# Kernel tuning notes

Measured on AMD Instinct MI355X. Metric: run time of the kernel, lower is better.

## Reference

```python
import jax, jax.numpy as jnp
import numpy as np

IN_F = 256
OUT_F = 256
ALPHA = 0.2  # leaky-relu slope
NEG_INF = -9e15


def setup_inputs() -> dict:
    key = jax.random.key(0)
    ks = jax.random.split(key, 8)
    N_e, N_kc = 10000, 2000
    exercise_h = jax.random.normal(ks[0], (N_e, IN_F), dtype=jnp.float32)
    kc_h = jax.random.normal(ks[1], (N_kc, IN_F), dtype=jnp.float32)
    adj = jax.random.randint(ks[2], (N_e, N_kc), 0, 2, dtype=jnp.int32)
    # parameters (kaiming-ish scaling)
    W1 = jax.random.normal(ks[3], (IN_F, OUT_F), dtype=jnp.float32) * np.sqrt(2.0 / IN_F)
    E = jax.random.normal(ks[4], (IN_F, OUT_F), dtype=jnp.float32) * np.sqrt(2.0 / IN_F)
    a = jax.random.normal(ks[5], (2 * OUT_F, 1), dtype=jnp.float32) * np.sqrt(2.0 / (2 * OUT_F))
    rd_w = jax.random.normal(ks[6], (OUT_F, 2 * OUT_F), dtype=jnp.float32) * np.sqrt(2.0 / (2 * OUT_F))
    rd_b = jnp.zeros((OUT_F,), dtype=jnp.float32)
    return {"exercise_h": exercise_h, "kc_h": kc_h, "adj": adj,
            "W1": W1, "E": E, "a": a, "rd_w": rd_w, "rd_b": rd_b}


def reference(exercise_h, kc_h, adj, W1, E, a, rd_w, rd_b):
    kc_Wh = kc_h @ W1            # [N_kc, D]
    ex_Wh = exercise_h @ W1      # [N_e, D]
    # a . concat(ex_Wh_i, kc_Wh_j) == a1.ex_Wh_i + a2.kc_Wh_j  (avoids [N_e,N_kc,2D] tensor)
    a1 = a[:OUT_F, 0]
    a2 = a[OUT_F:, 0]
    e = jax.nn.leaky_relu((ex_Wh @ a1)[:, None] + (kc_Wh @ a2)[None, :], negative_slope=ALPHA)  # [N_e, N_kc]
    logits = jnp.where(adj > 0, e, jnp.float32(NEG_INF))
    attention = jax.nn.softmax(logits, axis=1)
    new_kc = attention @ kc_Wh           # [N_e, D]
    ex_Eh = exercise_h @ E               # [N_e, D]
    feat = jnp.concatenate([new_kc, new_kc * ex_Eh], axis=1)  # [N_e, 2D]
    out = feat @ rd_w.T + rd_b
    return jax.nn.elu(out)
```

## Files before the change

kernel.cpp:

```cpp
#include <hip/hip_runtime.h>

#define N_E 10000
#define N_KC 2000
#define ALPHA 0.2f

typedef __attribute__((ext_vector_type(8))) short short8;
typedef __attribute__((ext_vector_type(4))) float f32x4;

__device__ float g_w1a1[256];
__device__ float g_t[2048];
__device__ __align__(16) unsigned short g_W1T_pk[16 * 8 * 512];
__device__ __align__(16) unsigned short g_ET_pk[16 * 8 * 512];
__device__ __align__(16) unsigned short g_rdw_pk[16 * 16 * 512];
__device__ __align__(16) unsigned short g_kcWh_pk[16 * 64 * 512];

__device__ __forceinline__ unsigned short f2bf(float f) {
  union { float f; unsigned int u; } v; v.f = f;
  unsigned int r = v.u + 0x7FFFu + ((v.u >> 16) & 1u);
  return (unsigned short)(r >> 16);
}

__device__ __forceinline__ void cvt_store4(float4 v, unsigned short* dst) {
  ushort4 o;
  o.x = f2bf(v.x); o.y = f2bf(v.y); o.z = f2bf(v.z); o.w = f2bf(v.w);
  *reinterpret_cast<ushort4*>(dst) = o;
}

__global__ __launch_bounds__(256) void prep_kernel(
    const float* __restrict__ W1, const float* __restrict__ E,
    const float* __restrict__ a, const float* __restrict__ rd_w) {
  int b = blockIdx.x, tid = threadIdx.x;
  if (b < 32) {
#pragma unroll
    for (int s2 = 0; s2 < 2; ++s2) {
      int sId = b * 512 + tid + s2 * 256;
      int ct = sId >> 10, rem = sId & 1023;
      int kt = rem >> 6, lane = rem & 63;
      int g = lane >> 4, r = lane & 15;
      const float* src = rd_w + (size_t)(ct * 16 + r) * 512 + kt * 32 + g * 8;
      unsigned short* dst = g_rdw_pk + (size_t)sId * 8;
      cvt_store4(*(const float4*)src, dst);
      cvt_store4(*(const float4*)(src + 4), dst + 4);
    }
  } else if (b < 48) {
#pragma unroll
    for (int s2 = 0; s2 < 2; ++s2) {
      int sId = (b - 32) * 512 + tid + s2 * 256;
      int ct = sId >> 9, rem = sId & 511;
      int kt = rem >> 6, lane = rem & 63;
      int g = lane >> 4, r = lane & 15;
      int col = ct * 16 + r, k = kt * 32 + g * 8;
      unsigned short* dst = g_W1T_pk + (size_t)sId * 8;
      ushort4 o0, o1;
      o0.x = f2bf(W1[(k + 0) * 256 + col]); o0.y = f2bf(W1[(k + 1) * 256 + col]);
      o0.z = f2bf(W1[(k + 2) * 256 + col]); o0.w = f2bf(W1[(k + 3) * 256 + col]);
      o1.x = f2bf(W1[(k + 4) * 256 + col]); o1.y = f2bf(W1[(k + 5) * 256 + col]);
      o1.z = f2bf(W1[(k + 6) * 256 + col]); o1.w = f2bf(W1[(k + 7) * 256 + col]);
      *(ushort4*)dst = o0; *(ushort4*)(dst + 4) = o1;
    }
  } else if (b < 64) {
#pragma unroll
    for (int s2 = 0; s2 < 2; ++s2) {
      int sId = (b - 48) * 512 + tid + s2 * 256;
      int ct = sId >> 9, rem = sId & 511;
      int kt = rem >> 6, lane = rem & 63;
      int g = lane >> 4, r = lane & 15;
      int col = ct * 16 + r, k = kt * 32 + g * 8;
      unsigned short* dst = g_ET_pk + (size_t)sId * 8;
      ushort4 o0, o1;
      o0.x = f2bf(E[(k + 0) * 256 + col]); o0.y = f2bf(E[(k + 1) * 256 + col]);
      o0.z = f2bf(E[(k + 2) * 256 + col]); o0.w = f2bf(E[(k + 3) * 256 + col]);
      o1.x = f2bf(E[(k + 4) * 256 + col]); o1.y = f2bf(E[(k + 5) * 256 + col]);
      o1.z = f2bf(E[(k + 6) * 256 + col]); o1.w = f2bf(E[(k + 7) * 256 + col]);
      *(ushort4*)dst = o0; *(ushort4*)(dst + 4) = o1;
    }
  } else if (b == 64) {
    float acc = 0.f;
    for (int q = 0; q < 64; ++q) {
      float4 wv = *(const float4*)(W1 + (size_t)tid * 256 + q * 4);
      float4 a4 = *(const float4*)(a + q * 4);
      acc += wv.x * a4.x + wv.y * a4.y + wv.z * a4.z + wv.w * a4.w;
    }
    g_w1a1[tid] = acc;
  } else {
    for (int idx = tid; idx < 16 * 2 * 512; idx += 256) {
      int ct = idx >> 10, rem = idx & 1023;
      int kt = 62 + (rem >> 9), off = rem & 511;
      g_kcWh_pk[((size_t)ct * 64 + kt) * 512 + off] = 0;
    }
    if (tid < 48) g_t[2000 + tid] = 0.f;
  }
}

__global__ __launch_bounds__(256) void kc_mfma_kernel(
    const float* __restrict__ kc_h, const float* __restrict__ a) {
  __shared__ float tred[4][4][4];
  int tid = threadIdx.x, lane = tid & 63, w = tid >> 6;
  int r = lane & 15, g = lane >> 4;
  int j0 = blockIdx.x * 16;
  f32x4 acc[4] = {{0.f,0.f,0.f,0.f},{0.f,0.f,0.f,0.f},
                  {0.f,0.f,0.f,0.f},{0.f,0.f,0.f,0.f}};
  for (int kk = 0; kk < 8; ++kk) {
    int k = kk * 32 + g * 8;
    const float* src = kc_h + (size_t)(j0 + r) * 256 + k;
    float4 x0 = *(const float4*)src, x1 = *(const float4*)(src + 4);
    short8 af = {(short)f2bf(x0.x), (short)f2bf(x0.y), (short)f2bf(x0.z),
                 (short)f2bf(x0.w), (short)f2bf(x1.x), (short)f2bf(x1.y),
                 (short)f2bf(x1.z), (short)f2bf(x1.w)};
#pragma unroll
    for (int n = 0; n < 4; ++n) {
      short8 bf = *(const short8*)(g_W1T_pk + ((size_t)(w * 4 + n) * 8 + kk) *
                                                  512 + lane * 8);
      acc[n] = __builtin_amdgcn_mfma_f32_16x16x32_bf16(af, bf, acc[n], 0, 0, 0);
    }
  }
  int j = j0 + g * 4;
  int kt = j >> 5, lsub = ((j >> 3) & 3) * 16 + r, sub = (g & 1) * 4;
#pragma unroll
  for (int n = 0; n < 4; ++n) {
    int ct = w * 4 + n;
    ushort4 o;
    o.x = f2bf(acc[n][0]); o.y = f2bf(acc[n][1]);
    o.z = f2bf(acc[n][2]); o.w = f2bf(acc[n][3]);
    *reinterpret_cast<ushort4*>(
        g_kcWh_pk + ((size_t)ct * 64 + kt) * 512 + lsub * 8 + sub) = o;
  }
  float a2v[4];
#pragma unroll
  for (int n = 0; n < 4; ++n) a2v[n] = a[256 + w * 64 + n * 16 + r];
  float tp[4];
#pragma unroll
  for (int q = 0; q < 4; ++q)
    tp[q] = acc[0][q] * a2v[0] + acc[1][q] * a2v[1] + acc[2][q] * a2v[2] +
            acc[3][q] * a2v[3];
#pragma unroll
  for (int off = 1; off < 16; off <<= 1)
#pragma unroll
    for (int q = 0; q < 4; ++q) tp[q] += __shfl_xor(tp[q], off, 64);
  if (r == 0)
#pragma unroll
    for (int q = 0; q < 4; ++q) tred[w][g][q] = tp[q];
  __syncthreads();
  if (tid < 16)
    g_t[j0 + tid] = tred[0][tid >> 2][tid & 3] + tred[1][tid >> 2][tid & 3] +
                    tred[2][tid >> 2][tid & 3] + tred[3][tid >> 2][tid & 3];
}

#define PSTR 136
#define FST 536
__global__ __launch_bounds__(512, 4) void main_kernel(
    const float* __restrict__ exh, const int* __restrict__ adj,
    const float* __restrict__ rd_b, float* __restrict__ out) {
  __shared__ __align__(16) unsigned char smem[41984];
  __shared__ float ds_part[8][32];
  __shared__ float red32[32];
  float* t_s = (float*)smem;
  unsigned short* p_s = (unsigned short*)(smem + 8192);
  unsigned short* exh_pk_s = (unsigned short*)(smem + 25600);
  unsigned short* feat_s = (unsigned short*)smem;

  int tid = threadIdx.x, w = tid >> 6, lane = tid & 63;
  int r = lane & 15, g = lane >> 4;
  int i0 = blockIdx.x * 32;
  int mh = w >> 2;
  int kw = w & 3;

  ((float4*)t_s)[tid] = ((const float4*)g_t)[tid];
  {
    const float* wsrc = g_w1a1 + w * 32 + g * 8;
    float4 w0 = *(const float4*)wsrc, w1 = *(const float4*)(wsrc + 4);
    float sp[2];
#pragma unroll
    for (int m = 0; m < 2; ++m) {
      int row = i0 + m * 16 + r; row = row < N_E ? row : N_E - 1;
      const float* xsrc = exh + (size_t)row * 256 + w * 32 + g * 8;
      float4 x0 = *(const float4*)xsrc, x1 = *(const float4*)(xsrc + 4);
      unsigned short* dst = exh_pk_s + m * 4096 + w * 512 + lane * 8;
      cvt_store4(x0, dst); cvt_store4(x1, dst + 4);
      sp[m] = x0.x * w0.x + x0.y * w0.y + x0.z * w0.z + x0.w * w0.w +
              x1.x * w1.x + x1.y * w1.y + x1.z * w1.z + x1.w * w1.w;
      sp[m] += __shfl_xor(sp[m], 16, 64);
      sp[m] += __shfl_xor(sp[m], 32, 64);
    }
    if (lane < 16) { ds_part[w][lane] = sp[0]; ds_part[w][16 + lane] = sp[1]; }
  }
  __syncthreads();
  if (tid < 32) {
    float sv = 0.f;
#pragma unroll
    for (int ww = 0; ww < 8; ++ww) sv += ds_part[ww][tid];
    red32[tid] = sv;
  }
  __syncthreads();
  float sv = red32[mh * 16 + r];
  int grow = i0 + mh * 16 + r; grow = grow < N_E ? grow : N_E - 1;
  const int* arow = adj + (size_t)grow * N_KC;

  f32x4 accP[2][2] = {{{0.f,0.f,0.f,0.f},{0.f,0.f,0.f,0.f}},
                      {{0.f,0.f,0.f,0.f},{0.f,0.f,0.f,0.f}}};
  float dsum = 0.f;

  auto gen = [&](int c) {
    int kk = c * 4 + kw;
    int c0 = kk * 32 + g * 8;
    int4 pk = {0, 0, 0, 0};
    if (kk < 63 && c0 < N_KC) {
      int4 a0 = *(const int4*)(arow + c0);
      int4 a1 = *(const int4*)(arow + c0 + 4);
      float4 t0 = *(const float4*)(t_s + c0);
      float4 t1 = *(const float4*)(t_s + c0 + 4);
      float tv[8] = {t0.x, t0.y, t0.z, t0.w, t1.x, t1.y, t1.z, t1.w};
      int av[8] = {a0.x, a0.y, a0.z, a0.w, a1.x, a1.y, a1.z, a1.w};
      unsigned ub[8];
#pragma unroll
      for (int j = 0; j < 8; ++j) {
        float x = sv + tv[j];
        float lx = fmaxf(x, ALPHA * x);
        float pv = (av[j] > 0) ? __expf(lx) : 0.f;
        dsum += pv;
        ub[j] = __float_as_uint(pv) + 0x8000u;
      }
      pk.x = (int)((ub[0] >> 16) | (ub[1] & 0xFFFF0000u));
      pk.y = (int)((ub[2] >> 16) | (ub[3] & 0xFFFF0000u));
      pk.z = (int)((ub[4] >> 16) | (ub[5] & 0xFFFF0000u));
      pk.w = (int)((ub[6] >> 16) | (ub[7] & 0xFFFF0000u));
    }
    *(int4*)(p_s + ((size_t)(c & 1) * 32 + mh * 16 + r) * PSTR + kw * 32 +
             g * 8) = pk;
  };

  auto mfma_chunk = [&](int c) {
    const unsigned short* pb = p_s + (size_t)(c & 1) * 32 * PSTR;
    const unsigned short* bb0 =
        g_kcWh_pk + ((size_t)(w * 2 + 0) * 64 + c * 4) * 512 + lane * 8;
    const unsigned short* bb1 =
        g_kcWh_pk + ((size_t)(w * 2 + 1) * 64 + c * 4) * 512 + lane * 8;
    short8 b0 = *(const short8*)bb0;
    short8 b1 = *(const short8*)bb1;
#pragma unroll
    for (int u = 0; u < 4; ++u) {
      short8 a0 = *(const short8*)(pb + (size_t)r * PSTR + u * 32 + g * 8);
      short8 a1 = *(const short8*)(pb + (size_t)(16 + r) * PSTR + u * 32 + g * 8);
      short8 nb0 = b0, nb1 = b1;
      if (u < 3) {
        nb0 = *(const short8*)(bb0 + (u + 1) * 512);
        nb1 = *(const short8*)(bb1 + (u + 1) * 512);
      }
      accP[0][0] = __builtin_amdgcn_mfma_f32_16x16x32_bf16(a0, b0, accP[0][0], 0, 0, 0);
      accP[1][0] = __builtin_amdgcn_mfma_f32_16x16x32_bf16(a1, b0, accP[1][0], 0, 0, 0);
      accP[0][1] = __builtin_amdgcn_mfma_f32_16x16x32_bf16(a0, b1, accP[0][1], 0, 0, 0);
      accP[1][1] = __builtin_amdgcn_mfma_f32_16x16x32_bf16(a1, b1, accP[1][1], 0, 0, 0);
      b0 = nb0; b1 = nb1;
    }
  };

  gen(0);
  __syncthreads();
  for (int c = 1; c < 16; ++c) {
    gen(c);
    mfma_chunk(c - 1);
    __syncthreads();
  }
  mfma_chunk(15);

  dsum += __shfl_xor(dsum, 16, 64);
  dsum += __shfl_xor(dsum, 32, 64);
  if (lane < 16) {
    ds_part[w][mh * 16 + lane] = dsum;
    ds_part[w][(1 - mh) * 16 + lane] = 0.f;
  }

  f32x4 accE[2][2] = {{{0.f,0.f,0.f,0.f},{0.f,0.f,0.f,0.f}},
                      {{0.f,0.f,0.f,0.f},{0.f,0.f,0.f,0.f}}};
#pragma unroll
  for (int kk = 0; kk < 8; ++kk) {
    short8 a0 = *(const short8*)(exh_pk_s + kk * 512 + lane * 8);
    short8 a1 = *(const short8*)(exh_pk_s + 4096 + kk * 512 + lane * 8);
#pragma unroll
    for (int n = 0; n < 2; ++n) {
      short8 bf = *(const short8*)(g_ET_pk + ((size_t)(w * 2 + n) * 8 + kk) *
                                                 512 + lane * 8);
      accE[0][n] = __builtin_amdgcn_mfma_f32_16x16x32_bf16(a0, bf, accE[0][n], 0, 0, 0);
      accE[1][n] = __builtin_amdgcn_mfma_f32_16x16x32_bf16(a1, bf, accE[1][n], 0, 0, 0);
    }
  }
  __syncthreads();
  if (tid < 32) {
    float s = 0.f;
#pragma unroll
    for (int ww = 0; ww < 8; ++ww) s += ds_part[ww][tid];
    red32[tid] = 1.f / fmaxf(s, 1e-30f);
  }
  __syncthreads();

  int c0e = w * 32;
#pragma unroll
  for (int m = 0; m < 2; ++m)
#pragma unroll
    for (int n = 0; n < 2; ++n) {
      int col = c0e + n * 16 + r;
#pragma unroll
      for (int q = 0; q < 4; ++q) {
        int row = m * 16 + g * 4 + q;
        float nk = accP[m][n][q] * red32[row];
        feat_s[(size_t)row * FST + col] = f2bf(nk);
        feat_s[(size_t)row * FST + 256 + col] = f2bf(nk * accE[m][n][q]);
      }
    }
  __syncthreads();

  f32x4 accO[2][2] = {{{0.f,0.f,0.f,0.f},{0.f,0.f,0.f,0.f}},
                      {{0.f,0.f,0.f,0.f},{0.f,0.f,0.f,0.f}}};
#pragma unroll
  for (int kt = 0; kt < 16; ++kt) {
    int k = kt * 32 + g * 8;
    short8 a0 = *(const short8*)(feat_s + (size_t)r * FST + k);
    short8 a1 = *(const short8*)(feat_s + (size_t)(16 + r) * FST + k);
#pragma unroll
    for (int n = 0; n < 2; ++n) {
      short8 bf = *(const short8*)(g_rdw_pk + ((size_t)(w * 2 + n) * 16 + kt) *
                                                  512 + lane * 8);
      accO[0][n] = __builtin_amdgcn_mfma_f32_16x16x32_bf16(a0, bf, accO[0][n], 0, 0, 0);
      accO[1][n] = __builtin_amdgcn_mfma_f32_16x16x32_bf16(a1, bf, accO[1][n], 0, 0, 0);
    }
  }
#pragma unroll
  for (int m = 0; m < 2; ++m) {
    if (i0 + m * 16 >= N_E) continue;
#pragma unroll
    for (int n = 0; n < 2; ++n) {
      int col = c0e + n * 16 + r;
      float bias = rd_b[col];
#pragma unroll
      for (int q = 0; q < 4; ++q) {
        int row = i0 + m * 16 + g * 4 + q;
        float x = accO[m][n][q] + bias;
        float res = x > 0.f ? x : (__expf(x) - 1.f);
        out[(size_t)row * 256 + col] = res;
      }
    }
  }
}

extern "C" void kernel_launch(void* const* d_in, const int* in_sizes, int n_in,
                              void* d_out, int out_size, void* d_ws,
                              size_t ws_size, hipStream_t stream) {
  const float* exh  = (const float*)d_in[0];
  const float* kc_h = (const float*)d_in[1];
  const int*   adj  = (const int*)d_in[2];
  const float* W1   = (const float*)d_in[3];
  const float* E    = (const float*)d_in[4];
  const float* a    = (const float*)d_in[5];
  const float* rd_w = (const float*)d_in[6];
  const float* rd_b = (const float*)d_in[7];
  float* out = (float*)d_out;

  prep_kernel<<<66, 256, 0, stream>>>(W1, E, a, rd_w);
  kc_mfma_kernel<<<N_KC / 16, 256, 0, stream>>>(kc_h, a);
  main_kernel<<<(N_E + 31) / 32, 512, 0, stream>>>(exh, adj, rd_b, out);
}
```

Baseline: 184.2 us.

## Shrink main kernel row tile to 16 and software-prefetch adjacency loads

Each block of the main kernel now handles 16 exercise rows instead of 32, doubling the grid and raising the launch-bounds occupancy target from 4 to 8 blocks. Every wave now walks the full K range in 8 chunks of 256 columns instead of the previous two-half split. The adjacency int4 loads are prefetched into registers one chunk ahead, so global-load latency overlaps the exp/pack and MFMA work. The cost is that the kcWh, E and rd_w B-fragments are each reused by only one 16-row M-tile, so global/L2 traffic for those weights per output row roughly doubles. The row clamp for N_E is also removed, which is safe only because 10000 divides evenly by 16.

```diff
diff --git a/kernel.cpp b/kernel.cpp
--- a/kernel.cpp
+++ b/kernel.cpp
@@ -146,71 +146,64 @@
                     tred[2][tid >> 2][tid & 3] + tred[3][tid >> 2][tid & 3];
 }
 
-#define PSTR 136
+#define PSTR 264
 #define FST 536
-__global__ __launch_bounds__(512, 4) void main_kernel(
+__global__ __launch_bounds__(512, 8) void main_kernel(
     const float* __restrict__ exh, const int* __restrict__ adj,
     const float* __restrict__ rd_b, float* __restrict__ out) {
-  __shared__ __align__(16) unsigned char smem[41984];
-  __shared__ float ds_part[8][32];
-  __shared__ float red32[32];
+  __shared__ __align__(16) unsigned char smem[33280];
+  __shared__ float ds_part[8][16];
+  __shared__ float red16[16];
   float* t_s = (float*)smem;
   unsigned short* p_s = (unsigned short*)(smem + 8192);
-  unsigned short* exh_pk_s = (unsigned short*)(smem + 25600);
+  unsigned short* exh_pk_s = (unsigned short*)(smem + 25088);
   unsigned short* feat_s = (unsigned short*)smem;
 
   int tid = threadIdx.x, w = tid >> 6, lane = tid & 63;
   int r = lane & 15, g = lane >> 4;
-  int i0 = blockIdx.x * 32;
-  int mh = w >> 2;
-  int kw = w & 3;
+  int i0 = blockIdx.x * 16;
+
+  const int* arow = adj + (size_t)(i0 + r) * N_KC;
+
+  int4 pa0 = *(const int4*)(arow + w * 32 + g * 8);
+  int4 pa1 = *(const int4*)(arow + w * 32 + g * 8 + 4);
 
   ((float4*)t_s)[tid] = ((const float4*)g_t)[tid];
   {
     const float* wsrc = g_w1a1 + w * 32 + g * 8;
     float4 w0 = *(const float4*)wsrc, w1 = *(const float4*)(wsrc + 4);
-    float sp[2];
-#pragma unroll
-    for (int m = 0; m < 2; ++m) {
-      int row = i0 + m * 16 + r; row = row < N_E ? row : N_E - 1;
-      const float* xsrc = exh + (size_t)row * 256 + w * 32 + g * 8;
-      float4 x0 = *(const float4*)xsrc, x1 = *(const float4*)(xsrc + 4);
-      unsigned short* dst = exh_pk_s + m * 4096 + w * 512 + lane * 8;
-      cvt_store4(x0, dst); cvt_store4(x1, dst + 4);
-      sp[m] = x0.x * w0.x + x0.y * w0.y + x0.z * w0.z + x0.w * w0.w +
-              x1.x * w1.x + x1.y * w1.y + x1.z * w1.z + x1.w * w1.w;
-      sp[m] += __shfl_xor(sp[m], 16, 64);
-      sp[m] += __shfl_xor(sp[m], 32, 64);
-    }
-    if (lane < 16) { ds_part[w][lane] = sp[0]; ds_part[w][16 + lane] = sp[1]; }
-  }
-  __syncthreads();
-  if (tid < 32) {
-    float sv = 0.f;
-#pragma unroll
-    for (int ww = 0; ww < 8; ++ww) sv += ds_part[ww][tid];
-    red32[tid] = sv;
-  }
-  __syncthreads();
-  float sv = red32[mh * 16 + r];
-  int grow = i0 + mh * 16 + r; grow = grow < N_E ? grow : N_E - 1;
-  const int* arow = adj + (size_t)grow * N_KC;
-
-  f32x4 accP[2][2] = {{{0.f,0.f,0.f,0.f},{0.f,0.f,0.f,0.f}},
-                      {{0.f,0.f,0.f,0.f},{0.f,0.f,0.f,0.f}}};
+    const float* xsrc = exh + (size_t)(i0 + r) * 256 + w * 32 + g * 8;
+    float4 x0 = *(const float4*)xsrc, x1 = *(const float4*)(xsrc + 4);
+    unsigned short* dst = exh_pk_s + w * 512 + lane * 8;
+    cvt_store4(x0, dst); cvt_store4(x1, dst + 4);
+    float sp = x0.x * w0.x + x0.y * w0.y + x0.z * w0.z + x0.w * w0.w +
+               x1.x * w1.x + x1.y * w1.y + x1.z * w1.z + x1.w * w1.w;
+    sp += __shfl_xor(sp, 16, 64);
+    sp += __shfl_xor(sp, 32, 64);
+    if (lane < 16) ds_part[w][lane] = sp;
+  }
+  __syncthreads();
+  if (tid < 16) {
+    float s = 0.f;
+#pragma unroll
+    for (int ww = 0; ww < 8; ++ww) s += ds_part[ww][tid];
+    red16[tid] = s;
+  }
+  __syncthreads();
+  float sv = red16[r];
+
+  f32x4 accP[2] = {{0.f,0.f,0.f,0.f},{0.f,0.f,0.f,0.f}};
   float dsum = 0.f;
 
-  auto gen = [&](int c) {
-    int kk = c * 4 + kw;
+  auto gen = [&](int c, int4 a0v, int4 a1v) {
+    int kk = c * 8 + w;
     int c0 = kk * 32 + g * 8;
     int4 pk = {0, 0, 0, 0};
     if (kk < 63 && c0 < N_KC) {
-      int4 a0 = *(const int4*)(arow + c0);
-      int4 a1 = *(const int4*)(arow + c0 + 4);
       float4 t0 = *(const float4*)(t_s + c0);
       float4 t1 = *(const float4*)(t_s + c0 + 4);
       float tv[8] = {t0.x, t0.y, t0.z, t0.w, t1.x, t1.y, t1.z, t1.w};
-      int av[8] = {a0.x, a0.y, a0.z, a0.w, a1.x, a1.y, a1.z, a1.w};
+      int av[8] = {a0v.x, a0v.y, a0v.z, a0v.w, a1v.x, a1v.y, a1v.z, a1v.w};
       unsigned ub[8];
 #pragma unroll
       for (int j = 0; j < 8; ++j) {
@@ -225,119 +218,98 @@
       pk.z = (int)((ub[4] >> 16) | (ub[5] & 0xFFFF0000u));
       pk.w = (int)((ub[6] >> 16) | (ub[7] & 0xFFFF0000u));
     }
-    *(int4*)(p_s + ((size_t)(c & 1) * 32 + mh * 16 + r) * PSTR + kw * 32 +
-             g * 8) = pk;
+    *(int4*)(p_s + ((size_t)((c & 1) * 16 + r)) * PSTR + w * 32 + g * 8) = pk;
   };
 
   auto mfma_chunk = [&](int c) {
-    const unsigned short* pb = p_s + (size_t)(c & 1) * 32 * PSTR;
-    const unsigned short* bb0 =
-        g_kcWh_pk + ((size_t)(w * 2 + 0) * 64 + c * 4) * 512 + lane * 8;
-    const unsigned short* bb1 =
-        g_kcWh_pk + ((size_t)(w * 2 + 1) * 64 + c * 4) * 512 + lane * 8;
-    short8 b0 = *(const short8*)bb0;
-    short8 b1 = *(const short8*)bb1;
-#pragma unroll
-    for (int u = 0; u < 4; ++u) {
-      short8 a0 = *(const short8*)(pb + (size_t)r * PSTR + u * 32 + g * 8);
-      short8 a1 = *(const short8*)(pb + (size_t)(16 + r) * PSTR + u * 32 + g * 8);
-      short8 nb0 = b0, nb1 = b1;
-      if (u < 3) {
-        nb0 = *(const short8*)(bb0 + (u + 1) * 512);
-        nb1 = *(const short8*)(bb1 + (u + 1) * 512);
+    const unsigned short* pb = p_s + (size_t)(c & 1) * 16 * PSTR;
+    const unsigned short* bb =
+        g_kcWh_pk + ((size_t)(w * 2) * 64 + c * 8) * 512 + lane * 8;
+#pragma unroll
+    for (int u = 0; u < 8; ++u) {
+      short8 av = *(const short8*)(pb + (size_t)r * PSTR + u * 32 + g * 8);
+      short8 b0 = *(const short8*)(bb + u * 512);
+      short8 b1 = *(const short8*)(bb + 64 * 512 + u * 512);
+      accP[0] = __builtin_amdgcn_mfma_f32_16x16x32_bf16(av, b0, accP[0], 0, 0, 0);
+      accP[1] = __builtin_amdgcn_mfma_f32_16x16x32_bf16(av, b1, accP[1], 0, 0, 0);
+    }
+  };
+
+  int4 na0 = {0, 0, 0, 0}, na1 = {0, 0, 0, 0};
+  for (int c = 0; c < 8; ++c) {
+    if (c < 7) {
+      int kk = (c + 1) * 8 + w, c0 = kk * 32 + g * 8;
+      if (kk < 63 && c0 < N_KC) {
+        na0 = *(const int4*)(arow + c0);
+        na1 = *(const int4*)(arow + c0 + 4);
       }
-      accP[0][0] = __builtin_amdgcn_mfma_f32_16x16x32_bf16(a0, b0, accP[0][0], 0, 0, 0);
-      accP[1][0] = __builtin_amdgcn_mfma_f32_16x16x32_bf16(a1, b0, accP[1][0], 0, 0, 0);
-      accP[0][1] = __builtin_amdgcn_mfma_f32_16x16x32_bf16(a0, b1, accP[0][1], 0, 0, 0);
-      accP[1][1] = __builtin_amdgcn_mfma_f32_16x16x32_bf16(a1, b1, accP[1][1], 0, 0, 0);
-      b0 = nb0; b1 = nb1;
-    }
-  };
-
-  gen(0);
-  __syncthreads();
-  for (int c = 1; c < 16; ++c) {
-    gen(c);
-    mfma_chunk(c - 1);
+    }
+    gen(c, pa0, pa1);
+    if (c > 0) mfma_chunk(c - 1);
     __syncthreads();
-  }
-  mfma_chunk(15);
+    pa0 = na0; pa1 = na1;
+  }
+  mfma_chunk(7);
 
   dsum += __shfl_xor(dsum, 16, 64);
   dsum += __shfl_xor(dsum, 32, 64);
-  if (lane < 16) {
-    ds_part[w][mh * 16 + lane] = dsum;
-    ds_part[w][(1 - mh) * 16 + lane] = 0.f;
-  }
-
-  f32x4 accE[2][2] = {{{0.f,0.f,0.f,0.f},{0.f,0.f,0.f,0.f}},
-                      {{0.f,0.f,0.f,0.f},{0.f,0.f,0.f,0.f}}};
+  if (lane < 16) ds_part[w][lane] = dsum;
+
+  f32x4 accE[2] = {{0.f,0.f,0.f,0.f},{0.f,0.f,0.f,0.f}};
 #pragma unroll
   for (int kk = 0; kk < 8; ++kk) {
     short8 a0 = *(const short8*)(exh_pk_s + kk * 512 + lane * 8);
-    short8 a1 = *(const short8*)(exh_pk_s + 4096 + kk * 512 + lane * 8);
 #pragma unroll
     for (int n = 0; n < 2; ++n) {
       short8 bf = *(const short8*)(g_ET_pk + ((size_t)(w * 2 + n) * 8 + kk) *
                                                  512 + lane * 8);
-      accE[0][n] = __builtin_amdgcn_mfma_f32_16x16x32_bf16(a0, bf, accE[0][n], 0, 0, 0);
-      accE[1][n] = __builtin_amdgcn_mfma_f32_16x16x32_bf16(a1, bf, accE[1][n], 0, 0, 0);
-    }
-  }
-  __syncthreads();
-  if (tid < 32) {
+      accE[n] = __builtin_amdgcn_mfma_f32_16x16x32_bf16(a0, bf, accE[n], 0, 0, 0);
+    }
+  }
+  __syncthreads();
+  if (tid < 16) {
     float s = 0.f;
 #pragma unroll
     for (int ww = 0; ww < 8; ++ww) s += ds_part[ww][tid];
-    red32[tid] = 1.f / fmaxf(s, 1e-30f);
-  }
-  __syncthreads();
-
-  int c0e = w * 32;
-#pragma unroll
-  for (int m = 0; m < 2; ++m)
-#pragma unroll
-    for (int n = 0; n < 2; ++n) {
-      int col = c0e + n * 16 + r;
-#pragma unroll
-      for (int q = 0; q < 4; ++q) {
-        int row = m * 16 + g * 4 + q;
-        float nk = accP[m][n][q] * red32[row];
-        feat_s[(size_t)row * FST + col] = f2bf(nk);
-        feat_s[(size_t)row * FST + 256 + col] = f2bf(nk * accE[m][n][q]);
-      }
-    }
-  __syncthreads();
-
-  f32x4 accO[2][2] = {{{0.f,0.f,0.f,0.f},{0.f,0.f,0.f,0.f}},
-                      {{0.f,0.f,0.f,0.f},{0.f,0.f,0.f,0.f}}};
+    red16[tid] = 1.f / fmaxf(s, 1e-30f);
+  }
+  __syncthreads();
+
+#pragma unroll
+  for (int n = 0; n < 2; ++n) {
+    int col = w * 32 + n * 16 + r;
+#pragma unroll
+    for (int q = 0; q < 4; ++q) {
+      int row = g * 4 + q;
+      float nk = accP[n][q] * red16[row];
+      feat_s[(size_t)row * FST + col] = f2bf(nk);
+      feat_s[(size_t)row * FST + 256 + col] = f2bf(nk * accE[n][q]);
+    }
+  }
+  __syncthreads();
+
+  f32x4 accO[2] = {{0.f,0.f,0.f,0.f},{0.f,0.f,0.f,0.f}};
 #pragma unroll
   for (int kt = 0; kt < 16; ++kt) {
     int k = kt * 32 + g * 8;
     short8 a0 = *(const short8*)(feat_s + (size_t)r * FST + k);
-    short8 a1 = *(const short8*)(feat_s + (size_t)(16 + r) * FST + k);
 #pragma unroll
     for (int n = 0; n < 2; ++n) {
       short8 bf = *(const short8*)(g_rdw_pk + ((size_t)(w * 2 + n) * 16 + kt) *
                                                   512 + lane * 8);
-      accO[0][n] = __builtin_amdgcn_mfma_f32_16x16x32_bf16(a0, bf, accO[0][n], 0, 0, 0);
-      accO[1][n] = __builtin_amdgcn_mfma_f32_16x16x32_bf16(a1, bf, accO[1][n], 0, 0, 0);
-    }
-  }
-#pragma unroll
-  for (int m = 0; m < 2; ++m) {
-    if (i0 + m * 16 >= N_E) continue;
-#pragma unroll
-    for (int n = 0; n < 2; ++n) {
-      int col = c0e + n * 16 + r;
-      float bias = rd_b[col];
-#pragma unroll
-      for (int q = 0; q < 4; ++q) {
-        int row = i0 + m * 16 + g * 4 + q;
-        float x = accO[m][n][q] + bias;
-        float res = x > 0.f ? x : (__expf(x) - 1.f);
-        out[(size_t)row * 256 + col] = res;
-      }
+      accO[n] = __builtin_amdgcn_mfma_f32_16x16x32_bf16(a0, bf, accO[n], 0, 0, 0);
+    }
+  }
+#pragma unroll
+  for (int n = 0; n < 2; ++n) {
+    int col = w * 32 + n * 16 + r;
+    float bias = rd_b[col];
+#pragma unroll
+    for (int q = 0; q < 4; ++q) {
+      int row = i0 + g * 4 + q;
+      float x = accO[n][q] + bias;
+      float res = x > 0.f ? x : (__expf(x) - 1.f);
+      out[(size_t)row * 256 + col] = res;
     }
   }
 }
@@ -357,5 +329,5 @@
 
   prep_kernel<<<66, 256, 0, stream>>>(W1, E, a, rd_w);
   kc_mfma_kernel<<<N_KC / 16, 256, 0, stream>>>(kc_h, a);
-  main_kernel<<<(N_E + 31) / 32, 512, 0, stream>>>(exh, adj, rd_b, out);
-}
+  main_kernel<<<(N_E + 15) / 16, 512, 0, stream>>>(exh, adj, rd_b, out);
+}
```

Measured after the change: 190.6 us. +3.5%, slower.

## Preload adjacency as ballot bitmasks and prefetch kcWh operands across chunks

Applied to the files above, without the earlier changes.

Before the attention loop, each wave reads its four adjacency rows with fully coalesced per-lane loads and compresses them into shared-memory bitmasks via __ballot. The generation step then reads one bitmask word instead of issuing scattered 32-byte int4 global loads per chunk. The P tile is also stored directly in MFMA operand layout, dropping the padded stride, and the kcWh B fragments for the next chunk are prefetched one iteration ahead. This targets the latency-bound adjacency streaming inside the compute loop. In exchange it adds a serial up-front load phase and about 8 KB of extra shared memory, which may lower occupancy.

```diff
diff --git a/kernel.cpp b/kernel.cpp
--- a/kernel.cpp
+++ b/kernel.cpp
@@ -146,17 +146,17 @@
                     tred[2][tid >> 2][tid & 3] + tred[3][tid >> 2][tid & 3];
 }
 
-#define PSTR 136
 #define FST 536
 __global__ __launch_bounds__(512, 4) void main_kernel(
     const float* __restrict__ exh, const int* __restrict__ adj,
     const float* __restrict__ rd_b, float* __restrict__ out) {
-  __shared__ __align__(16) unsigned char smem[41984];
+  __shared__ __align__(16) unsigned char smem[40960];
+  __shared__ unsigned int bits_s[32][66];
   __shared__ float ds_part[8][32];
   __shared__ float red32[32];
   float* t_s = (float*)smem;
-  unsigned short* p_s = (unsigned short*)(smem + 8192);
-  unsigned short* exh_pk_s = (unsigned short*)(smem + 25600);
+  unsigned short* p_pk = (unsigned short*)(smem + 8192);
+  unsigned short* exh_pk_s = (unsigned short*)(smem + 24576);
   unsigned short* feat_s = (unsigned short*)smem;
 
   int tid = threadIdx.x, w = tid >> 6, lane = tid & 63;
@@ -184,6 +184,46 @@
     }
     if (lane < 16) { ds_part[w][lane] = sp[0]; ds_part[w][16 + lane] = sp[1]; }
   }
+
+  {
+    const int* ar0; const int* ar1; const int* ar2; const int* ar3;
+    {
+      int q0 = i0 + w * 4 + 0; q0 = q0 < N_E ? q0 : N_E - 1;
+      int q1 = i0 + w * 4 + 1; q1 = q1 < N_E ? q1 : N_E - 1;
+      int q2 = i0 + w * 4 + 2; q2 = q2 < N_E ? q2 : N_E - 1;
+      int q3 = i0 + w * 4 + 3; q3 = q3 < N_E ? q3 : N_E - 1;
+      ar0 = adj + (size_t)q0 * N_KC; ar1 = adj + (size_t)q1 * N_KC;
+      ar2 = adj + (size_t)q2 * N_KC; ar3 = adj + (size_t)q3 * N_KC;
+    }
+#pragma unroll 2
+    for (int ch = 0; ch < 32; ++ch) {
+      int c = ch * 64 + lane;
+      bool inb = c < N_KC;
+      int v0 = inb ? ar0[c] : 0;
+      int v1 = inb ? ar1[c] : 0;
+      int v2 = inb ? ar2[c] : 0;
+      int v3 = inb ? ar3[c] : 0;
+      unsigned long long m0 = __ballot(v0 > 0);
+      unsigned long long m1 = __ballot(v1 > 0);
+      unsigned long long m2 = __ballot(v2 > 0);
+      unsigned long long m3 = __ballot(v3 > 0);
+      if (lane < 2) {
+        int sh = lane * 32;
+        bits_s[w * 4 + 0][ch * 2 + lane] = (unsigned int)(m0 >> sh);
+        bits_s[w * 4 + 1][ch * 2 + lane] = (unsigned int)(m1 >> sh);
+        bits_s[w * 4 + 2][ch * 2 + lane] = (unsigned int)(m2 >> sh);
+        bits_s[w * 4 + 3][ch * 2 + lane] = (unsigned int)(m3 >> sh);
+      }
+    }
+  }
+
+  const unsigned short* bb0 =
+      g_kcWh_pk + ((size_t)(w * 2 + 0) * 64) * 512 + lane * 8;
+  const unsigned short* bb1 =
+      g_kcWh_pk + ((size_t)(w * 2 + 1) * 64) * 512 + lane * 8;
+  short8 bp0 = *(const short8*)bb0;
+  short8 bp1 = *(const short8*)bb1;
+
   __syncthreads();
   if (tid < 32) {
     float sv = 0.f;
@@ -193,8 +233,6 @@
   }
   __syncthreads();
   float sv = red32[mh * 16 + r];
-  int grow = i0 + mh * 16 + r; grow = grow < N_E ? grow : N_E - 1;
-  const int* arow = adj + (size_t)grow * N_KC;
 
   f32x4 accP[2][2] = {{{0.f,0.f,0.f,0.f},{0.f,0.f,0.f,0.f}},
                       {{0.f,0.f,0.f,0.f},{0.f,0.f,0.f,0.f}}};
@@ -202,49 +240,39 @@
 
   auto gen = [&](int c) {
     int kk = c * 4 + kw;
+    unsigned int bw = bits_s[mh * 16 + r][kk];
+    unsigned int byte = (bw >> (g * 8)) & 0xFFu;
     int c0 = kk * 32 + g * 8;
-    int4 pk = {0, 0, 0, 0};
-    if (kk < 63 && c0 < N_KC) {
-      int4 a0 = *(const int4*)(arow + c0);
-      int4 a1 = *(const int4*)(arow + c0 + 4);
-      float4 t0 = *(const float4*)(t_s + c0);
-      float4 t1 = *(const float4*)(t_s + c0 + 4);
-      float tv[8] = {t0.x, t0.y, t0.z, t0.w, t1.x, t1.y, t1.z, t1.w};
-      int av[8] = {a0.x, a0.y, a0.z, a0.w, a1.x, a1.y, a1.z, a1.w};
-      unsigned ub[8];
-#pragma unroll
-      for (int j = 0; j < 8; ++j) {
-        float x = sv + tv[j];
-        float lx = fmaxf(x, ALPHA * x);
-        float pv = (av[j] > 0) ? __expf(lx) : 0.f;
-        dsum += pv;
-        ub[j] = __float_as_uint(pv) + 0x8000u;
-      }
-      pk.x = (int)((ub[0] >> 16) | (ub[1] & 0xFFFF0000u));
-      pk.y = (int)((ub[2] >> 16) | (ub[3] & 0xFFFF0000u));
-      pk.z = (int)((ub[4] >> 16) | (ub[5] & 0xFFFF0000u));
-      pk.w = (int)((ub[6] >> 16) | (ub[7] & 0xFFFF0000u));
-    }
-    *(int4*)(p_s + ((size_t)(c & 1) * 32 + mh * 16 + r) * PSTR + kw * 32 +
-             g * 8) = pk;
+    float4 t0 = *(const float4*)(t_s + c0);
+    float4 t1 = *(const float4*)(t_s + c0 + 4);
+    float tv[8] = {t0.x, t0.y, t0.z, t0.w, t1.x, t1.y, t1.z, t1.w};
+    unsigned ub[8];
+#pragma unroll
+    for (int j = 0; j < 8; ++j) {
+      float x = sv + tv[j];
+      float lx = fmaxf(x, ALPHA * x);
+      float pv = ((byte >> j) & 1u) ? __expf(lx) : 0.f;
+      dsum += pv;
+      ub[j] = __float_as_uint(pv) + 0x8000u;
+    }
+    int4 pk;
+    pk.x = (int)((ub[0] >> 16) | (ub[1] & 0xFFFF0000u));
+    pk.y = (int)((ub[2] >> 16) | (ub[3] & 0xFFFF0000u));
+    pk.z = (int)((ub[4] >> 16) | (ub[5] & 0xFFFF0000u));
+    pk.w = (int)((ub[6] >> 16) | (ub[7] & 0xFFFF0000u));
+    *(int4*)(p_pk + ((size_t)((c & 1) * 2 + mh) * 4 + kw) * 512 + lane * 8) = pk;
   };
 
-  auto mfma_chunk = [&](int c) {
-    const unsigned short* pb = p_s + (size_t)(c & 1) * 32 * PSTR;
-    const unsigned short* bb0 =
-        g_kcWh_pk + ((size_t)(w * 2 + 0) * 64 + c * 4) * 512 + lane * 8;
-    const unsigned short* bb1 =
-        g_kcWh_pk + ((size_t)(w * 2 + 1) * 64 + c * 4) * 512 + lane * 8;
-    short8 b0 = *(const short8*)bb0;
-    short8 b1 = *(const short8*)bb1;
+  auto mfma_chunk = [&](int c, short8 b0, short8 b1) {
+    const unsigned short* pb = p_pk + (size_t)(c & 1) * 4096;
 #pragma unroll
     for (int u = 0; u < 4; ++u) {
-      short8 a0 = *(const short8*)(pb + (size_t)r * PSTR + u * 32 + g * 8);
-      short8 a1 = *(const short8*)(pb + (size_t)(16 + r) * PSTR + u * 32 + g * 8);
+      short8 a0 = *(const short8*)(pb + (size_t)u * 512 + lane * 8);
+      short8 a1 = *(const short8*)(pb + (size_t)(4 + u) * 512 + lane * 8);
       short8 nb0 = b0, nb1 = b1;
       if (u < 3) {
-        nb0 = *(const short8*)(bb0 + (u + 1) * 512);
-        nb1 = *(const short8*)(bb1 + (u + 1) * 512);
+        nb0 = *(const short8*)(bb0 + (size_t)(c * 4 + u + 1) * 512);
+        nb1 = *(const short8*)(bb1 + (size_t)(c * 4 + u + 1) * 512);
       }
       accP[0][0] = __builtin_amdgcn_mfma_f32_16x16x32_bf16(a0, b0, accP[0][0], 0, 0, 0);
       accP[1][0] = __builtin_amdgcn_mfma_f32_16x16x32_bf16(a1, b0, accP[1][0], 0, 0, 0);
@@ -257,11 +285,14 @@
   gen(0);
   __syncthreads();
   for (int c = 1; c < 16; ++c) {
+    short8 np0 = *(const short8*)(bb0 + (size_t)(c * 4) * 512);
+    short8 np1 = *(const short8*)(bb1 + (size_t)(c * 4) * 512);
     gen(c);
-    mfma_chunk(c - 1);
+    mfma_chunk(c - 1, bp0, bp1);
     __syncthreads();
-  }
-  mfma_chunk(15);
+    bp0 = np0; bp1 = np1;
+  }
+  mfma_chunk(15, bp0, bp1);
 
   dsum += __shfl_xor(dsum, 16, 64);
   dsum += __shfl_xor(dsum, 32, 64);
```

New measurement: 209.4 us. 13.7% more time.

## Split fused attention kernel into separate P-generation and GEMM kernels

Applied to the files above, without the earlier changes.

The fused main kernel, which interleaved softmax-probability generation with MFMA on a double-buffered shared tile, is split in two. The first kernel streams adj, computes the bf16 probabilities and row inverse sums, and writes them to a global buffer. The second kernel reads them back for the attention GEMM and the feature/output GEMMs. This removes per-chunk block barriers and lets each phase run at its own occupancy, at the cost of an extra kernel launch and a round trip of about 40 MB of bf16 probabilities through global memory.

```diff
diff --git a/kernel.cpp b/kernel.cpp
--- a/kernel.cpp
+++ b/kernel.cpp
@@ -13,6 +13,8 @@
 __device__ __align__(16) unsigned short g_ET_pk[16 * 8 * 512];
 __device__ __align__(16) unsigned short g_rdw_pk[16 * 16 * 512];
 __device__ __align__(16) unsigned short g_kcWh_pk[16 * 64 * 512];
+__device__ __align__(16) unsigned short g_P_pk[626u * 63 * 512];
+__device__ float g_inv[10016];
 
 __device__ __forceinline__ unsigned short f2bf(float f) {
   union { float f; unsigned int u; } v; v.f = f;
@@ -146,67 +148,52 @@
                     tred[2][tid >> 2][tid & 3] + tred[3][tid >> 2][tid & 3];
 }
 
-#define PSTR 136
-#define FST 536
-__global__ __launch_bounds__(512, 4) void main_kernel(
-    const float* __restrict__ exh, const int* __restrict__ adj,
-    const float* __restrict__ rd_b, float* __restrict__ out) {
-  __shared__ __align__(16) unsigned char smem[41984];
-  __shared__ float ds_part[8][32];
-  __shared__ float red32[32];
-  float* t_s = (float*)smem;
-  unsigned short* p_s = (unsigned short*)(smem + 8192);
-  unsigned short* exh_pk_s = (unsigned short*)(smem + 25600);
-  unsigned short* feat_s = (unsigned short*)smem;
-
-  int tid = threadIdx.x, w = tid >> 6, lane = tid & 63;
+__global__ __launch_bounds__(256) void p_gen_kernel(
+    const float* __restrict__ exh, const int* __restrict__ adj) {
+  __shared__ float t_s[2048];
+  __shared__ float sv_s[16];
+  __shared__ float ds_red[4][16];
+  int tid = threadIdx.x, lane = tid & 63, q = tid >> 6;
+  int i0 = blockIdx.x * 16;
+
+  ((float4*)t_s)[tid] = ((const float4*)g_t)[tid];
+  ((float4*)t_s)[tid + 256] = ((const float4*)g_t)[tid + 256];
+
+  {
+    int row = tid >> 4, seg = tid & 15;
+    const float* xsrc = exh + (size_t)(i0 + row) * 256 + seg * 16;
+    const float* wsrc = g_w1a1 + seg * 16;
+    float sp = 0.f;
+#pragma unroll
+    for (int j = 0; j < 4; ++j) {
+      float4 x = *(const float4*)(xsrc + j * 4);
+      float4 wv = *(const float4*)(wsrc + j * 4);
+      sp += x.x * wv.x + x.y * wv.y + x.z * wv.z + x.w * wv.w;
+    }
+    sp += __shfl_xor(sp, 1, 64);
+    sp += __shfl_xor(sp, 2, 64);
+    sp += __shfl_xor(sp, 4, 64);
+    sp += __shfl_xor(sp, 8, 64);
+    if (seg == 0) sv_s[row] = sp;
+  }
+  __syncthreads();
+
   int r = lane & 15, g = lane >> 4;
-  int i0 = blockIdx.x * 32;
-  int mh = w >> 2;
-  int kw = w & 3;
-
-  ((float4*)t_s)[tid] = ((const float4*)g_t)[tid];
-  {
-    const float* wsrc = g_w1a1 + w * 32 + g * 8;
-    float4 w0 = *(const float4*)wsrc, w1 = *(const float4*)(wsrc + 4);
-    float sp[2];
-#pragma unroll
-    for (int m = 0; m < 2; ++m) {
-      int row = i0 + m * 16 + r; row = row < N_E ? row : N_E - 1;
-      const float* xsrc = exh + (size_t)row * 256 + w * 32 + g * 8;
-      float4 x0 = *(const float4*)xsrc, x1 = *(const float4*)(xsrc + 4);
-      unsigned short* dst = exh_pk_s + m * 4096 + w * 512 + lane * 8;
-      cvt_store4(x0, dst); cvt_store4(x1, dst + 4);
-      sp[m] = x0.x * w0.x + x0.y * w0.y + x0.z * w0.z + x0.w * w0.w +
-              x1.x * w1.x + x1.y * w1.y + x1.z * w1.z + x1.w * w1.w;
-      sp[m] += __shfl_xor(sp[m], 16, 64);
-      sp[m] += __shfl_xor(sp[m], 32, 64);
-    }
-    if (lane < 16) { ds_part[w][lane] = sp[0]; ds_part[w][16 + lane] = sp[1]; }
-  }
-  __syncthreads();
-  if (tid < 32) {
-    float sv = 0.f;
-#pragma unroll
-    for (int ww = 0; ww < 8; ++ww) sv += ds_part[ww][tid];
-    red32[tid] = sv;
-  }
-  __syncthreads();
-  float sv = red32[mh * 16 + r];
-  int grow = i0 + mh * 16 + r; grow = grow < N_E ? grow : N_E - 1;
-  const int* arow = adj + (size_t)grow * N_KC;
-
-  f32x4 accP[2][2] = {{{0.f,0.f,0.f,0.f},{0.f,0.f,0.f,0.f}},
-                      {{0.f,0.f,0.f,0.f},{0.f,0.f,0.f,0.f}}};
+  float sv = sv_s[r];
+  const int* arow = adj + (size_t)(i0 + r) * N_KC;
+  unsigned short* pb = g_P_pk + (size_t)blockIdx.x * 63 * 512 + lane * 8;
   float dsum = 0.f;
 
-  auto gen = [&](int c) {
-    int kk = c * 4 + kw;
-    int c0 = kk * 32 + g * 8;
-    int4 pk = {0, 0, 0, 0};
-    if (kk < 63 && c0 < N_KC) {
-      int4 a0 = *(const int4*)(arow + c0);
-      int4 a1 = *(const int4*)(arow + c0 + 4);
+#pragma unroll
+  for (int m = 0; m < 16; ++m) {
+    int kk = m * 4 + q;
+    if (kk < 63) {
+      int c0 = kk * 32 + g * 8;
+      int4 a0 = {0, 0, 0, 0}, a1 = {0, 0, 0, 0};
+      if (c0 + 8 <= N_KC) {
+        a0 = *(const int4*)(arow + c0);
+        a1 = *(const int4*)(arow + c0 + 4);
+      }
       float4 t0 = *(const float4*)(t_s + c0);
       float4 t1 = *(const float4*)(t_s + c0 + 4);
       float tv[8] = {t0.x, t0.y, t0.z, t0.w, t1.x, t1.y, t1.z, t1.w};
@@ -220,55 +207,76 @@
         dsum += pv;
         ub[j] = __float_as_uint(pv) + 0x8000u;
       }
+      int4 pk;
       pk.x = (int)((ub[0] >> 16) | (ub[1] & 0xFFFF0000u));
       pk.y = (int)((ub[2] >> 16) | (ub[3] & 0xFFFF0000u));
       pk.z = (int)((ub[4] >> 16) | (ub[5] & 0xFFFF0000u));
       pk.w = (int)((ub[6] >> 16) | (ub[7] & 0xFFFF0000u));
-    }
-    *(int4*)(p_s + ((size_t)(c & 1) * 32 + mh * 16 + r) * PSTR + kw * 32 +
-             g * 8) = pk;
-  };
-
-  auto mfma_chunk = [&](int c) {
-    const unsigned short* pb = p_s + (size_t)(c & 1) * 32 * PSTR;
-    const unsigned short* bb0 =
-        g_kcWh_pk + ((size_t)(w * 2 + 0) * 64 + c * 4) * 512 + lane * 8;
-    const unsigned short* bb1 =
-        g_kcWh_pk + ((size_t)(w * 2 + 1) * 64 + c * 4) * 512 + lane * 8;
-    short8 b0 = *(const short8*)bb0;
-    short8 b1 = *(const short8*)bb1;
-#pragma unroll
-    for (int u = 0; u < 4; ++u) {
-      short8 a0 = *(const short8*)(pb + (size_t)r * PSTR + u * 32 + g * 8);
-      short8 a1 = *(const short8*)(pb + (size_t)(16 + r) * PSTR + u * 32 + g * 8);
-      short8 nb0 = b0, nb1 = b1;
-      if (u < 3) {
-        nb0 = *(const short8*)(bb0 + (u + 1) * 512);
-        nb1 = *(const short8*)(bb1 + (u + 1) * 512);
-      }
-      accP[0][0] = __builtin_amdgcn_mfma_f32_16x16x32_bf16(a0, b0, accP[0][0], 0, 0, 0);
-      accP[1][0] = __builtin_amdgcn_mfma_f32_16x16x32_bf16(a1, b0, accP[1][0], 0, 0, 0);
-      accP[0][1] = __builtin_amdgcn_mfma_f32_16x16x32_bf16(a0, b1, accP[0][1], 0, 0, 0);
-      accP[1][1] = __builtin_amdgcn_mfma_f32_16x16x32_bf16(a1, b1, accP[1][1], 0, 0, 0);
-      b0 = nb0; b1 = nb1;
-    }
-  };
-
-  gen(0);
-  __syncthreads();
-  for (int c = 1; c < 16; ++c) {
-    gen(c);
-    mfma_chunk(c - 1);
-    __syncthreads();
-  }
-  mfma_chunk(15);
+      *(int4*)(pb + (size_t)kk * 512) = pk;
+    }
+  }
 
   dsum += __shfl_xor(dsum, 16, 64);
   dsum += __shfl_xor(dsum, 32, 64);
-  if (lane < 16) {
-    ds_part[w][mh * 16 + lane] = dsum;
-    ds_part[w][(1 - mh) * 16 + lane] = 0.f;
-  }
+  if (lane < 16) ds_red[q][lane] = dsum;
+  __syncthreads();
+  if (tid < 16) {
+    float s = ds_red[0][tid] + ds_red[1][tid] + ds_red[2][tid] + ds_red[3][tid];
+    g_inv[i0 + tid] = 1.f / fmaxf(s, 1e-30f);
+  }
+}
+
+#define FST 536
+__global__ __launch_bounds__(512, 4) void g_gemm_kernel(
+    const float* __restrict__ exh, const float* __restrict__ rd_b,
+    float* __restrict__ out) {
+  __shared__ __align__(16) unsigned char smem[34816];
+  __shared__ float inv_s[32];
+  unsigned short* exh_pk_s = (unsigned short*)smem;
+  unsigned short* feat_s = (unsigned short*)smem;
+
+  int tid = threadIdx.x, w = tid >> 6, lane = tid & 63;
+  int r = lane & 15, g = lane >> 4;
+  int i0 = blockIdx.x * 32;
+
+  {
+#pragma unroll
+    for (int m = 0; m < 2; ++m) {
+      int row = i0 + m * 16 + r; row = row < N_E ? row : N_E - 1;
+      const float* xsrc = exh + (size_t)row * 256 + w * 32 + g * 8;
+      float4 x0 = *(const float4*)xsrc, x1 = *(const float4*)(xsrc + 4);
+      unsigned short* dst = exh_pk_s + m * 4096 + w * 512 + lane * 8;
+      cvt_store4(x0, dst); cvt_store4(x1, dst + 4);
+    }
+  }
+  if (tid < 32) {
+    int row = i0 + tid;
+    inv_s[tid] = g_inv[row < N_E ? row : 0];
+  }
+
+  f32x4 accP[2][2] = {{{0.f,0.f,0.f,0.f},{0.f,0.f,0.f,0.f}},
+                      {{0.f,0.f,0.f,0.f},{0.f,0.f,0.f,0.f}}};
+  const unsigned short* pa0 =
+      g_P_pk + (size_t)(blockIdx.x * 2 + 0) * 63 * 512 + lane * 8;
+  const unsigned short* pa1 =
+      g_P_pk + (size_t)(blockIdx.x * 2 + 1) * 63 * 512 + lane * 8;
+  const unsigned short* bb0 =
+      g_kcWh_pk + (size_t)(w * 2 + 0) * 64 * 512 + lane * 8;
+  const unsigned short* bb1 =
+      g_kcWh_pk + (size_t)(w * 2 + 1) * 64 * 512 + lane * 8;
+#pragma unroll 7
+  for (int kk = 0; kk < 63; ++kk) {
+    short8 a0 = *(const short8*)(pa0 + (size_t)kk * 512);
+    short8 a1 = *(const short8*)(pa1 + (size_t)kk * 512);
+    short8 b0 = *(const short8*)(bb0 + (size_t)kk * 512);
+    short8 b1 = *(const short8*)(bb1 + (size_t)kk * 512);
+    accP[0][0] = __builtin_amdgcn_mfma_f32_16x16x32_bf16(a0, b0, accP[0][0], 0, 0, 0);
+    accP[1][0] = __builtin_amdgcn_mfma_f32_16x16x32_bf16(a1, b0, accP[1][0], 0, 0, 0);
+    accP[0][1] = __builtin_amdgcn_mfma_f32_16x16x32_bf16(a0, b1, accP[0][1], 0, 0, 0);
+    accP[1][1] = __builtin_amdgcn_mfma_f32_16x16x32_bf16(a1, b1, accP[1][1], 0, 0, 0);
+  }
+
+  __syncthreads();
 
   f32x4 accE[2][2] = {{{0.f,0.f,0.f,0.f},{0.f,0.f,0.f,0.f}},
                       {{0.f,0.f,0.f,0.f},{0.f,0.f,0.f,0.f}}};
@@ -285,13 +293,6 @@
     }
   }
   __syncthreads();
-  if (tid < 32) {
-    float s = 0.f;
-#pragma unroll
-    for (int ww = 0; ww < 8; ++ww) s += ds_part[ww][tid];
-    red32[tid] = 1.f / fmaxf(s, 1e-30f);
-  }
-  __syncthreads();
 
   int c0e = w * 32;
 #pragma unroll
@@ -300,11 +301,11 @@
     for (int n = 0; n < 2; ++n) {
       int col = c0e + n * 16 + r;
 #pragma unroll
-      for (int q = 0; q < 4; ++q) {
-        int row = m * 16 + g * 4 + q;
-        float nk = accP[m][n][q] * red32[row];
+      for (int q2 = 0; q2 < 4; ++q2) {
+        int row = m * 16 + g * 4 + q2;
+        float nk = accP[m][n][q2] * inv_s[row];
         feat_s[(size_t)row * FST + col] = f2bf(nk);
-        feat_s[(size_t)row * FST + 256 + col] = f2bf(nk * accE[m][n][q]);
+        feat_s[(size_t)row * FST + 256 + col] = f2bf(nk * accE[m][n][q2]);
       }
     }
   __syncthreads();
@@ -332,9 +333,9 @@
       int col = c0e + n * 16 + r;
       float bias = rd_b[col];
 #pragma unroll
-      for (int q = 0; q < 4; ++q) {
-        int row = i0 + m * 16 + g * 4 + q;
-        float x = accO[m][n][q] + bias;
+      for (int q2 = 0; q2 < 4; ++q2) {
+        int row = i0 + m * 16 + g * 4 + q2;
+        float x = accO[m][n][q2] + bias;
         float res = x > 0.f ? x : (__expf(x) - 1.f);
         out[(size_t)row * 256 + col] = res;
       }
@@ -357,5 +358,6 @@
 
   prep_kernel<<<66, 256, 0, stream>>>(W1, E, a, rd_w);
   kc_mfma_kernel<<<N_KC / 16, 256, 0, stream>>>(kc_h, a);
-  main_kernel<<<(N_E + 31) / 32, 512, 0, stream>>>(exh, adj, rd_b, out);
-}
+  p_gen_kernel<<<N_E / 16, 256, 0, stream>>>(exh, adj);
+  g_gemm_kernel<<<(N_E + 31) / 32, 512, 0, stream>>>(exh, rd_b, out);
+}
```

New measurement: 222.6 us. 1.21x slower.
